# Performance work log

Hardware: AMD Instinct MI355X
Metric: run time of the kernel (lower is better)

## Reference

```python
import jax, jax.numpy as jnp
import numpy as np
import math

B, D, E = 32768, 256, 8          # batch, feature dim (shape=[256]), num_steps experts
T_TOTAL = 1.0
H_STEP = T_TOTAL / E             # self.h
EIGMIN, EIGINIT, EIGMAX = -1.0, 0.0, 1.0
LOGIT_099 = math.log(0.99 / 0.01)


def setup_inputs() -> dict:
    key = jax.random.key(0)
    k_t, k_y, k_w1, k_w2 = jax.random.split(key, 4)
    std = 1.0 / math.sqrt(D)     # xavier-ish init for expert weights
    return {
        "t": jax.random.uniform(k_t, (B,), dtype=jnp.float32),            # times in [0, T)
        "y": jax.random.normal(k_y, (B, D), dtype=jnp.float32),
        "W1": jax.random.normal(k_w1, (E, D, D), dtype=jnp.float32) * std,
        "b1": jnp.zeros((E, D), dtype=jnp.float32),
        "W2": jax.random.normal(k_w2, (E, D, D), dtype=jnp.float32) * std,
        "b2": jnp.zeros((E, D), dtype=jnp.float32),
        "scales": jnp.full((1, D), LOGIT_099, dtype=jnp.float32),         # learn_scales=False init
        "shifta": jnp.asarray(LOGIT_099, dtype=jnp.float32),
        "shiftb": jnp.asarray(LOGIT_099, dtype=jnp.float32),
    }


def reference(t, y, W1, b1, W2, b2, scales, shifta, shiftb):
    # t2ind: clamp(int(t / h), max=E-1)
    ind = jnp.minimum((t / H_STEP).astype(jnp.int32), E - 1)            # [B]
    # per-sample dispatch to expert F[i] (2-layer MLP), grouped as masked
    # dense batched GEMMs per expert (E is a small fixed set)
    f = jnp.zeros_like(y)
    for e in range(E):
        h_e = jnp.tanh(jnp.einsum('bd,kd->bk', y, W1[e]) + b1[e])       # [B, D]
        f_e = jnp.einsum('bd,kd->bk', h_e, W2[e]) + b2[e]               # [B, D]
        f = jnp.where((ind == e)[:, None], f_e, f)
    # sigmoid-scale / affine-combine epilogue
    f = jax.nn.sigmoid(scales) * f
    a = EIGINIT + jax.nn.sigmoid(shifta) * (EIGMIN - EIGINIT)
    b = EIGINIT + jax.nn.sigmoid(shiftb) * (EIGMAX - EIGINIT)
    return 0.5 * ((b - a) * f + (a + b) * y)
```

## Files before the change

kernel.cpp:

```cpp
#include <hip/hip_runtime.h>

#define BATCH 32768
#define DIM   256
#define NEXP  8
#define MT    32
#define STRIDE 264

typedef __bf16 bf16x8 __attribute__((ext_vector_type(8)));
typedef __bf16 bf16x4 __attribute__((ext_vector_type(4)));
typedef float  f32x16 __attribute__((ext_vector_type(16)));

static __device__ __forceinline__ float sigmoid_f(float x) {
    return __builtin_amdgcn_rcpf(1.f + __expf(-x));
}
static __device__ __forceinline__ float tanh_f(float x) {
    return 1.f - 2.f * __builtin_amdgcn_rcpf(__expf(2.f * x) + 1.f);
}

__global__ void prep_kernel(const float* __restrict__ W1, const float* __restrict__ W2,
                            const float* __restrict__ t,
                            bf16x8* __restrict__ W1p, bf16x8* __restrict__ W2p,
                            int* __restrict__ cursor, int* __restrict__ idxb) {
    const int b = blockIdx.x;
    if (b < 256) {
        const int tid = b * 256 + threadIdx.x;
        const int nl = tid & 31;
        const int kh = (tid >> 5) & 1;
        const int ks = (tid >> 6) & 15;
        const int entt = tid >> 10;
        const int col = ((entt & 7) << 5) | nl;
        const int e   = entt >> 3;
        const long src = ((long)(e << 8 | col) << 8) + (ks << 4) + (kh << 3);
        const float4 a0 = *(const float4*)(W1 + src);
        const float4 a1 = *(const float4*)(W1 + src + 4);
        const float4 c0 = *(const float4*)(W2 + src);
        const float4 c1 = *(const float4*)(W2 + src + 4);
        bf16x8 w1, w2;
        w1[0] = (__bf16)a0.x; w1[1] = (__bf16)a0.y; w1[2] = (__bf16)a0.z; w1[3] = (__bf16)a0.w;
        w1[4] = (__bf16)a1.x; w1[5] = (__bf16)a1.y; w1[6] = (__bf16)a1.z; w1[7] = (__bf16)a1.w;
        w2[0] = (__bf16)c0.x; w2[1] = (__bf16)c0.y; w2[2] = (__bf16)c0.z; w2[3] = (__bf16)c0.w;
        w2[4] = (__bf16)c1.x; w2[5] = (__bf16)c1.y; w2[6] = (__bf16)c1.z; w2[7] = (__bf16)c1.w;
        W1p[tid] = w1;
        W2p[tid] = w2;
    } else {
        __shared__ int h[NEXP], base[NEXP];
        if (threadIdx.x < NEXP) h[threadIdx.x] = 0;
        __syncthreads();
        const int i = (b - 256) * 256 + threadIdx.x;
        const int e = min((int)(t[i] * 8.0f), NEXP - 1);
        const int lr = atomicAdd(&h[e], 1);
        __syncthreads();
        if (threadIdx.x < NEXP)
            base[threadIdx.x] = atomicAdd(&cursor[threadIdx.x], h[threadIdx.x]);
        __syncthreads();
        idxb[e * BATCH + base[e] + lr] = i;
    }
}

__global__ void __launch_bounds__(256, 4)
mlp_kernel(const float* __restrict__ y,
           const float* __restrict__ scales,
           const float* __restrict__ shifta,
           const float* __restrict__ shiftb,
           const float* __restrict__ b1,
           const float* __restrict__ b2,
           const bf16x8* __restrict__ W1p,
           const bf16x8* __restrict__ W2p,
           const int* __restrict__ cnt,
           const int* __restrict__ idxb,
           float* __restrict__ out) {
    __shared__ __bf16 ab[MT * STRIDE];
    __shared__ int rows[MT];

    const int tx   = threadIdx.x;
    const int wave = tx >> 6;
    const int lane = tx & 63;
    const int nl   = lane & 31;
    const int kh   = lane >> 5;
    const int nbase = wave * 64;

    int c[NEXP], tp[NEXP + 1];
    tp[0] = 0;
#pragma unroll
    for (int e = 0; e < NEXP; ++e) {
        c[e] = cnt[e];
        tp[e + 1] = tp[e] + ((c[e] + MT - 1) >> 5);
    }
    const int total = tp[NEXP];

    const float sa = sigmoid_f(shifta[0]);
    const float sb = sigmoid_f(shiftb[0]);
    const float av = -sa;
    const float bvv = sb;
    const float k1 = 0.5f * (bvv - av);
    const float k2 = 0.5f * (av + bvv);
    const bool needy = (k2 != 0.0f);

    for (int tile = blockIdx.x; tile < total; tile += gridDim.x) {
        int e = 0;
#pragma unroll
        for (int j = 0; j < NEXP; ++j) if (tile >= tp[j + 1]) e = j + 1;
        const int rbase = (tile - tp[e]) * MT;
        const int nrows = min(MT, c[e] - rbase);
        const int* idx_e = idxb + e * BATCH;

        __syncthreads();
#pragma unroll
        for (int pass = 0; pass < 8; ++pass) {
            const int r  = pass * 4 + wave;
            const int rr = min(r, nrows - 1);
            const int g  = idx_e[rbase + rr];
            if (lane == 0) rows[r] = (r < nrows) ? g : -1;
            const float4 v = *(const float4*)(y + (long)g * DIM + lane * 4);
            bf16x4 w;
            w[0] = (__bf16)v.x; w[1] = (__bf16)v.y; w[2] = (__bf16)v.z; w[3] = (__bf16)v.w;
            *(bf16x4*)(ab + r * STRIDE + lane * 4) = w;
        }
        __syncthreads();

        const __bf16* apt = ab + nl * STRIDE + kh * 8;

        const bf16x8* w1p = W1p + ((e << 3) << 10) + (((nbase >> 5) << 10)) + lane;
        f32x16 acc[2] = {};
#pragma unroll
        for (int ks = 0; ks < 16; ++ks) {
            bf16x8 a = *(const bf16x8*)(apt + ks * 16);
#pragma unroll
            for (int ni = 0; ni < 2; ++ni) {
                bf16x8 bb = w1p[(ni << 10) + (ks << 6)];
                acc[ni] = __builtin_amdgcn_mfma_f32_32x32x16_bf16(a, bb, acc[ni], 0, 0, 0);
            }
        }
        __syncthreads();

#pragma unroll
        for (int ni = 0; ni < 2; ++ni) {
            const int n = nbase + ni * 32 + nl;
            const float b1v = b1[(e << 8) | n];
#pragma unroll
            for (int r = 0; r < 16; ++r) {
                const int row = (r & 3) + ((r >> 2) << 3) + (kh << 2);
                ab[row * STRIDE + n] = (__bf16)tanh_f(acc[ni][r] + b1v);
            }
        }
        __syncthreads();

        const bf16x8* w2p = W2p + ((e << 3) << 10) + (((nbase >> 5) << 10)) + lane;
        f32x16 acc2[2] = {};
#pragma unroll
        for (int ks = 0; ks < 16; ++ks) {
            bf16x8 a = *(const bf16x8*)(apt + ks * 16);
#pragma unroll
            for (int ni = 0; ni < 2; ++ni) {
                bf16x8 bb = w2p[(ni << 10) + (ks << 6)];
                acc2[ni] = __builtin_amdgcn_mfma_f32_32x32x16_bf16(a, bb, acc2[ni], 0, 0, 0);
            }
        }

#pragma unroll
        for (int ni = 0; ni < 2; ++ni) {
            const int n = nbase + ni * 32 + nl;
            const float c1  = k1 * sigmoid_f(scales[n]);
            const float b2v = b2[(e << 8) | n];
#pragma unroll
            for (int r = 0; r < 16; ++r) {
                const int row = (r & 3) + ((r >> 2) << 3) + (kh << 2);
                const int g = rows[row];
                if (g >= 0) {
                    float res = c1 * (acc2[ni][r] + b2v);
                    if (needy) res += k2 * y[(long)g * DIM + n];
                    out[(long)g * DIM + n] = res;
                }
            }
        }
    }
}

extern "C" void kernel_launch(void* const* d_in, const int* in_sizes, int n_in,
                              void* d_out, int out_size, void* d_ws, size_t ws_size,
                              hipStream_t stream) {
    const float* t      = (const float*)d_in[0];
    const float* y      = (const float*)d_in[1];
    const float* W1     = (const float*)d_in[2];
    const float* b1     = (const float*)d_in[3];
    const float* W2     = (const float*)d_in[4];
    const float* b2     = (const float*)d_in[5];
    const float* scales = (const float*)d_in[6];
    const float* shifta = (const float*)d_in[7];
    const float* shiftb = (const float*)d_in[8];
    float* out = (float*)d_out;

    char* ws = (char*)d_ws;
    int* cursor = (int*)ws;
    int* idxb   = (int*)(ws + 256);
    bf16x8* W1p = (bf16x8*)(ws + 256 + NEXP * BATCH * 4);
    bf16x8* W2p = W1p + 65536;

    hipMemsetAsync(cursor, 0, 32, stream);
    prep_kernel<<<384, 256, 0, stream>>>(W1, W2, t, W1p, W2p, cursor, idxb);
    mlp_kernel<<<1032, 256, 0, stream>>>(y, scales, shifta, shiftb, b1, b2,
                                         W1p, W2p, cursor, idxb, out);
}
```

Before: 133.0 us.

## Double row tile to 64 so each weight fragment feeds two MFMAs

The row tile per block grows from 32 to 64 rows, and each wave now issues two MFMAs per loaded weight fragment, which halves weight reads from global memory per row. The grid shrinks to match. The prep kernel is also reworked to read the fp32 weights contiguously and scatter to the packed layout, so its loads coalesce. The cost is more accumulator registers, larger shared memory per block (64x264 bf16), and more padding waste in each expert's last tile.

```diff
diff --git a/kernel.cpp b/kernel.cpp
--- a/kernel.cpp
+++ b/kernel.cpp
@@ -3,7 +3,7 @@
 #define BATCH 32768
 #define DIM   256
 #define NEXP  8
-#define MT    32
+#define MT    64
 #define STRIDE 264
 
 typedef __bf16 bf16x8 __attribute__((ext_vector_type(8)));
@@ -24,13 +24,11 @@
     const int b = blockIdx.x;
     if (b < 256) {
         const int tid = b * 256 + threadIdx.x;
-        const int nl = tid & 31;
-        const int kh = (tid >> 5) & 1;
-        const int ks = (tid >> 6) & 15;
-        const int entt = tid >> 10;
-        const int col = ((entt & 7) << 5) | nl;
-        const int e   = entt >> 3;
-        const long src = ((long)(e << 8 | col) << 8) + (ks << 4) + (kh << 3);
+        const int kh  = tid & 1;
+        const int ks  = (tid >> 1) & 15;
+        const int col = (tid >> 5) & 255;
+        const int e   = tid >> 13;
+        const long src = (long)tid * 8;
         const float4 a0 = *(const float4*)(W1 + src);
         const float4 a1 = *(const float4*)(W1 + src + 4);
         const float4 c0 = *(const float4*)(W2 + src);
@@ -40,8 +38,9 @@
         w1[4] = (__bf16)a1.x; w1[5] = (__bf16)a1.y; w1[6] = (__bf16)a1.z; w1[7] = (__bf16)a1.w;
         w2[0] = (__bf16)c0.x; w2[1] = (__bf16)c0.y; w2[2] = (__bf16)c0.z; w2[3] = (__bf16)c0.w;
         w2[4] = (__bf16)c1.x; w2[5] = (__bf16)c1.y; w2[6] = (__bf16)c1.z; w2[7] = (__bf16)c1.w;
-        W1p[tid] = w1;
-        W2p[tid] = w2;
+        const int dst = (e << 13) | ((col >> 5) << 10) | (ks << 6) | (kh << 5) | (col & 31);
+        W1p[dst] = w1;
+        W2p[dst] = w2;
     } else {
         __shared__ int h[NEXP], base[NEXP];
         if (threadIdx.x < NEXP) h[threadIdx.x] = 0;
@@ -84,7 +83,7 @@
 #pragma unroll
     for (int e = 0; e < NEXP; ++e) {
         c[e] = cnt[e];
-        tp[e + 1] = tp[e] + ((c[e] + MT - 1) >> 5);
+        tp[e + 1] = tp[e] + ((c[e] + MT - 1) >> 6);
     }
     const int total = tp[NEXP];
 
@@ -106,7 +105,7 @@
 
         __syncthreads();
 #pragma unroll
-        for (int pass = 0; pass < 8; ++pass) {
+        for (int pass = 0; pass < 16; ++pass) {
             const int r  = pass * 4 + wave;
             const int rr = min(r, nrows - 1);
             const int g  = idx_e[rbase + rr];
@@ -118,17 +117,20 @@
         }
         __syncthreads();
 
-        const __bf16* apt = ab + nl * STRIDE + kh * 8;
-
-        const bf16x8* w1p = W1p + ((e << 3) << 10) + (((nbase >> 5) << 10)) + lane;
-        f32x16 acc[2] = {};
+        const __bf16* apt0 = ab + nl * STRIDE + kh * 8;
+        const __bf16* apt1 = ab + (32 + nl) * STRIDE + kh * 8;
+
+        const bf16x8* w1p = W1p + (e << 13) + ((nbase >> 5) << 10) + lane;
+        f32x16 acc[2][2] = {};
 #pragma unroll
         for (int ks = 0; ks < 16; ++ks) {
-            bf16x8 a = *(const bf16x8*)(apt + ks * 16);
+            bf16x8 a0 = *(const bf16x8*)(apt0 + ks * 16);
+            bf16x8 a1 = *(const bf16x8*)(apt1 + ks * 16);
 #pragma unroll
             for (int ni = 0; ni < 2; ++ni) {
                 bf16x8 bb = w1p[(ni << 10) + (ks << 6)];
-                acc[ni] = __builtin_amdgcn_mfma_f32_32x32x16_bf16(a, bb, acc[ni], 0, 0, 0);
+                acc[0][ni] = __builtin_amdgcn_mfma_f32_32x32x16_bf16(a0, bb, acc[0][ni], 0, 0, 0);
+                acc[1][ni] = __builtin_amdgcn_mfma_f32_32x32x16_bf16(a1, bb, acc[1][ni], 0, 0, 0);
             }
         }
         __syncthreads();
@@ -138,22 +140,27 @@
             const int n = nbase + ni * 32 + nl;
             const float b1v = b1[(e << 8) | n];
 #pragma unroll
-            for (int r = 0; r < 16; ++r) {
-                const int row = (r & 3) + ((r >> 2) << 3) + (kh << 2);
-                ab[row * STRIDE + n] = (__bf16)tanh_f(acc[ni][r] + b1v);
-            }
-        }
-        __syncthreads();
-
-        const bf16x8* w2p = W2p + ((e << 3) << 10) + (((nbase >> 5) << 10)) + lane;
-        f32x16 acc2[2] = {};
+            for (int mi = 0; mi < 2; ++mi) {
+#pragma unroll
+                for (int r = 0; r < 16; ++r) {
+                    const int row = mi * 32 + (r & 3) + ((r >> 2) << 3) + (kh << 2);
+                    ab[row * STRIDE + n] = (__bf16)tanh_f(acc[mi][ni][r] + b1v);
+                }
+            }
+        }
+        __syncthreads();
+
+        const bf16x8* w2p = W2p + (e << 13) + ((nbase >> 5) << 10) + lane;
+        f32x16 acc2[2][2] = {};
 #pragma unroll
         for (int ks = 0; ks < 16; ++ks) {
-            bf16x8 a = *(const bf16x8*)(apt + ks * 16);
+            bf16x8 a0 = *(const bf16x8*)(apt0 + ks * 16);
+            bf16x8 a1 = *(const bf16x8*)(apt1 + ks * 16);
 #pragma unroll
             for (int ni = 0; ni < 2; ++ni) {
                 bf16x8 bb = w2p[(ni << 10) + (ks << 6)];
-                acc2[ni] = __builtin_amdgcn_mfma_f32_32x32x16_bf16(a, bb, acc2[ni], 0, 0, 0);
+                acc2[0][ni] = __builtin_amdgcn_mfma_f32_32x32x16_bf16(a0, bb, acc2[0][ni], 0, 0, 0);
+                acc2[1][ni] = __builtin_amdgcn_mfma_f32_32x32x16_bf16(a1, bb, acc2[1][ni], 0, 0, 0);
             }
         }
 
@@ -163,13 +170,16 @@
             const float c1  = k1 * sigmoid_f(scales[n]);
             const float b2v = b2[(e << 8) | n];
 #pragma unroll
-            for (int r = 0; r < 16; ++r) {
-                const int row = (r & 3) + ((r >> 2) << 3) + (kh << 2);
-                const int g = rows[row];
-                if (g >= 0) {
-                    float res = c1 * (acc2[ni][r] + b2v);
-                    if (needy) res += k2 * y[(long)g * DIM + n];
-                    out[(long)g * DIM + n] = res;
+            for (int mi = 0; mi < 2; ++mi) {
+#pragma unroll
+                for (int r = 0; r < 16; ++r) {
+                    const int row = mi * 32 + (r & 3) + ((r >> 2) << 3) + (kh << 2);
+                    const int g = rows[row];
+                    if (g >= 0) {
+                        float res = c1 * (acc2[mi][ni][r] + b2v);
+                        if (needy) res += k2 * y[(long)g * DIM + n];
+                        out[(long)g * DIM + n] = res;
+                    }
                 }
             }
         }
@@ -198,6 +208,6 @@
 
     hipMemsetAsync(cursor, 0, 32, stream);
     prep_kernel<<<384, 256, 0, stream>>>(W1, W2, t, W1p, W2p, cursor, idxb);
-    mlp_kernel<<<1032, 256, 0, stream>>>(y, scales, shifta, shiftb, b1, b2,
-                                         W1p, W2p, cursor, idxb, out);
-}
+    mlp_kernel<<<520, 256, 0, stream>>>(y, scales, shifta, shiftb, b1, b2,
+                                        W1p, W2p, cursor, idxb, out);
+}
```

After: 138.2 us. 3.9% more time.
